# Performance work log

Hardware: AMD Instinct MI355X
Metric: run time of the kernel (lower is better)

Reference implementation:

```python
import jax, jax.numpy as jnp
import numpy as np

BLOCKS = (1, 2, 3, 4)      # (block_size, offset=0) from max_block_size=4
BLOCK_MULT = 12            # lcm(1,2,3,4)
DS = 4                     # downsample_factor
MAX_BS = 4                 # max block size (also pos_conv kernel size)
DIM = 512
VOCAB = 256


def _masked_mean(t, m, axis):
    # t: [..., L, D], m: [..., L] bool -> mean over axis with mask, 0 where empty
    mf = m[..., None].astype(t.dtype)
    num = jnp.sum(t * mf, axis=axis)
    tot = jnp.sum(mf, axis=axis)
    mean = num / jnp.clip(tot, 1.0)
    return jnp.where(tot == 0.0, jnp.zeros_like(mean), mean)


def setup_inputs() -> dict:
    key = jax.random.key(0)
    ks = jax.random.split(key, 8)
    B, S = 8, 2048
    return {
        "x": jax.random.randint(ks[0], (B, S), 0, VOCAB),
        "mask": jnp.ones((B, S), dtype=bool),
        "emb": jax.random.normal(ks[1], (VOCAB, DIM), jnp.float32) * 0.02,
        "dw_w": jax.random.normal(ks[2], (MAX_BS, 1, DIM), jnp.float32) * 0.1,   # depthwise kernel (W, I=1, O=DIM)
        "dw_b": jnp.zeros((DIM,), jnp.float32),
        "pw_w": jax.random.normal(ks[3], (1, DIM, DIM), jnp.float32) * 0.03,     # pointwise 1x1 conv
        "pw_b": jnp.zeros((DIM,), jnp.float32),
        "score_w": jax.random.normal(ks[4], (DIM, 1), jnp.float32) * 0.05,
        "score_b": jnp.zeros((1,), jnp.float32),
    }


def reference(x, mask, emb, dw_w, dw_b, pw_w, pw_b, score_w, score_b):
    B, S = x.shape
    D = DIM
    trunc = ((S + DS - 1) // DS) * DS  # next_divisible_length(S, DS); equals S here

    h = emb[x]                                              # [B,S,D]
    h = jnp.pad(h, ((0, 0), (0, MAX_BS - 1), (0, 0)))       # right pad for VALID conv
    dn = jax.lax.conv_dimension_numbers(h.shape, dw_w.shape, ('NWC', 'WIO', 'NWC'))
    h = jax.lax.conv_general_dilated(h, dw_w, (1,), 'VALID',
                                     dimension_numbers=dn,
                                     feature_group_count=D) + dw_b  # depthwise -> [B,S,D]
    h = jnp.einsum('bsd,de->bse', h, pw_w[0]) + pw_b                # pointwise

    # pad seq to multiple of lcm of block sizes
    Sp = ((h.shape[1] + BLOCK_MULT - 1) // BLOCK_MULT) * BLOCK_MULT
    pad = Sp - h.shape[1]
    h = jnp.pad(h, ((0, 0), (0, pad), (0, 0)))
    m = jnp.pad(mask.astype(bool), ((0, 0), (0, pad)), constant_values=False)

    reprs, rmasks = [], []
    for bsz in BLOCKS:  # fixed small set of block sizes (offset=0 for all)
        nb = Sp // bsz
        g = h.reshape(B, nb, bsz, D)
        mg = m.reshape(B, nb, bsz)
        r = _masked_mean(g, mg, axis=2)                       # [B,nb,D]
        reprs.append(jnp.repeat(r, bsz, axis=1))              # [B,Sp,D]
        rmasks.append(jnp.repeat(jnp.any(mg, axis=-1), bsz, axis=1))

    block_reprs = jnp.stack(reprs, axis=2)    # [B,Sp,M,D]
    block_masks = jnp.stack(rmasks, axis=2)   # [B,Sp,M]

    scores = (block_reprs @ score_w)[..., 0] + score_b[0]     # [B,Sp,M]
    max_neg = -jnp.finfo(scores.dtype).max
    scores = jnp.where(block_masks, scores, max_neg)
    scores = jnp.nan_to_num(jax.nn.softmax(scores, axis=2), nan=0.0)

    # consensus attention over positions
    sim = jnp.einsum('bim,bjm->bij', scores, scores)          # [B,Sp,Sp]
    cm = m[:, :, None] & m[:, None, :]
    sim = jnp.where(cm, sim, max_neg)
    attn = jnp.nan_to_num(jax.nn.softmax(sim, axis=-1), nan=0.0)
    scores = jnp.einsum('bij,bjm->bim', attn, scores)

    out = jnp.einsum('bsmd,bsm->bsd', block_reprs, scores)    # weighted combine
    out = out[:, :trunc]
    mt = m[:, :trunc]

    nl = trunc // DS
    xb = out.reshape(B, nl, DS, D)
    mb = mt.reshape(B, nl, DS)
    out = _masked_mean(xb, mb, axis=2)                        # [B, S/DS, D]
    out_mask = jnp.any(mb, axis=-1)
    return out, out_mask
```

## Files before the change

kernel.cpp:

```cpp
#include <hip/hip_runtime.h>
#include <stdint.h>
#include <stddef.h>

typedef __bf16 bf16_t;
typedef bf16_t bf16x4v __attribute__((ext_vector_type(4)));
typedef bf16_t bf16x8v __attribute__((ext_vector_type(8)));
typedef float  f32x4   __attribute__((ext_vector_type(4)));

#define NBATCH 8
#define SEQ    2048
#define DIM    512
#define SP     2052
#define NB2    1026
#define NB3    684
#define NB4    513
#define NL     512
#define NJC    8
#define JCH    257

static __device__ __forceinline__ f32x4 ldbf4(const bf16_t* p) {
  bf16x4v v = *(const bf16x4v*)p;
  f32x4 r;
  r.x = (float)v[0]; r.y = (float)v[1]; r.z = (float)v[2]; r.w = (float)v[3];
  return r;
}
static __device__ __forceinline__ void stbf4(bf16_t* p, f32x4 v) {
  bf16x4v o;
  o[0] = (bf16_t)v.x; o[1] = (bf16_t)v.y; o[2] = (bf16_t)v.z; o[3] = (bf16_t)v.w;
  *(bf16x4v*)p = o;
}

static __device__ __forceinline__ void gload_lds16(const void* g, void* l) {
  __builtin_amdgcn_global_load_lds(
      (const __attribute__((address_space(1))) void*)g,
      (__attribute__((address_space(3))) void*)l, 16, 0, 0);
}

#define GA_WT   256
#define GA_MASK 65
#define GA_A    (NBATCH * SEQ / 2)
__global__ __launch_bounds__(256) void kA_prep(
    const float* __restrict__ pw, bf16_t* __restrict__ Wt,
    const void* __restrict__ mraw, float* __restrict__ mask01,
    const int* __restrict__ x, const float* __restrict__ emb,
    const float* __restrict__ dww, const float* __restrict__ dwb,
    bf16_t* __restrict__ A) {
  const int bx = blockIdx.x, t = threadIdx.x;
  if (bx < GA_WT) {
    __shared__ float T[32][33];
    int ti = bx >> 4, tj = bx & 15;
    int r = t >> 3, c0 = (t & 7) * 4;
    f32x4 v = *(const f32x4*)(pw + (size_t)(ti * 32 + r) * DIM + tj * 32 + c0);
    T[c0 + 0][r] = v.x; T[c0 + 1][r] = v.y;
    T[c0 + 2][r] = v.z; T[c0 + 3][r] = v.w;
    __syncthreads();
    bf16x4v o;
    o[0] = (bf16_t)T[r][c0 + 0]; o[1] = (bf16_t)T[r][c0 + 1];
    o[2] = (bf16_t)T[r][c0 + 2]; o[3] = (bf16_t)T[r][c0 + 3];
    *(bf16x4v*)(Wt + (size_t)(tj * 32 + r) * DIM + ti * 32 + c0) = o;
    return;
  }
  if (bx < GA_WT + GA_MASK) {
    int idx = (bx - GA_WT) * 256 + t;
    if (idx >= NBATCH * SP) return;
    int b = idx / SP, s = idx - b * SP;
    const unsigned char* mb = (const unsigned char*)mraw;
    int u8 = 0;
#pragma unroll
    for (int i = 0; i < 64; i++)
      if ((i & 3) != 0 && mb[i] != 0) u8 = 1;
    float v = 0.f;
    if (s < SEQ) {
      int mi = b * SEQ + s;
      int nz = u8 ? (mb[mi] != 0) : (((const int*)mraw)[mi] != 0);
      v = nz ? 1.f : 0.f;
    }
    mask01[idx] = v;
    return;
  }
  int rp = bx - (GA_WT + GA_MASK);
  int row = rp * 2 + (t >> 7);
  int b = row >> 11, s = row & 2047;
  int d0 = (t & 127) * 4;
  f32x4 acc = *(const f32x4*)(dwb + d0);
#pragma unroll
  for (int tt = 0; tt < 4; tt++) {
    int sp = s + tt;
    if (sp < SEQ) {
      int v = x[b * SEQ + sp];
      f32x4 e = *(const f32x4*)(emb + (size_t)v * DIM + d0);
      f32x4 w = *(const f32x4*)(dww + tt * DIM + d0);
      acc += e * w;
    }
  }
  stbf4(A + (size_t)row * DIM + d0, acc);
}

#define BM 64
#define BN 128
#define BK 32
__global__ __launch_bounds__(256) void k2_gemm(
    const bf16_t* __restrict__ A, const bf16_t* __restrict__ Bt,
    const float* __restrict__ bias, bf16_t* __restrict__ H) {
  __shared__ __align__(16) bf16_t As[BM * BK];
  __shared__ __align__(16) bf16_t Bs[BN * BK];
  const int t = threadIdx.x;
  const int bid = blockIdx.x;
  const int xcd = bid & 7, loc = bid >> 3;
  const int mt = xcd * 32 + (loc >> 2);
  const int nt = loc & 3;
  const int m0 = mt * BM, n0 = nt * BN;
  const int lane = t & 63, wave = t >> 6;
  const int wm = (wave & 1) * 32, wn = (wave >> 1) * 64;
  const int mloc = lane & 15, quad = lane >> 4;

  f32x4 acc[2][4] = {};

  char* asd  = (char*)As + t * 16;
  char* bsd1 = (char*)Bs + t * 16;
  char* bsd2 = (char*)Bs + (t + 256) * 16;
  const int ar = t >> 2,           ak = (t & 3) * 8;
  const int br1 = t >> 2,          bk1 = (t & 3) * 8;
  const int br2 = (t + 256) >> 2,  bk2 = (t & 3) * 8;

  for (int k0 = 0; k0 < 512; k0 += BK) {
    gload_lds16(A + (size_t)(m0 + ar) * DIM + k0 + ak, asd);
    gload_lds16(Bt + (size_t)(n0 + br1) * DIM + k0 + bk1, bsd1);
    gload_lds16(Bt + (size_t)(n0 + br2) * DIM + k0 + bk2, bsd2);
    __syncthreads();
    bf16x8v af[2], bfr[4];
#pragma unroll
    for (int i = 0; i < 2; i++)
      af[i] = *(const bf16x8v*)&As[(wm + i * 16 + mloc) * BK + quad * 8];
#pragma unroll
    for (int i = 0; i < 4; i++)
      bfr[i] = *(const bf16x8v*)&Bs[(wn + i * 16 + mloc) * BK + quad * 8];
#pragma unroll
    for (int mi = 0; mi < 2; mi++)
#pragma unroll
      for (int ni = 0; ni < 4; ni++)
        acc[mi][ni] = __builtin_amdgcn_mfma_f32_16x16x32_bf16(
            af[mi], bfr[ni], acc[mi][ni], 0, 0, 0);
    __syncthreads();
  }
#pragma unroll
  for (int ni = 0; ni < 4; ni++) {
    int col = n0 + wn + ni * 16 + mloc;
    float bv = bias[col];
#pragma unroll
    for (int mi = 0; mi < 2; mi++) {
      int rbase = m0 + wm + mi * 16 + quad * 4;
#pragma unroll
      for (int r = 0; r < 4; r++)
        H[(size_t)(rbase + r) * DIM + col] = (bf16_t)(acc[mi][ni][r] + bv);
    }
  }
}

__global__ __launch_bounds__(128) void kB_levels(
    const bf16_t* __restrict__ H, const float* __restrict__ mask01,
    const float* __restrict__ sw, const float* __restrict__ sbp,
    bf16_t* __restrict__ R2, bf16_t* __restrict__ R3, bf16_t* __restrict__ R4,
    float* __restrict__ P) {
  const int b = blockIdx.x, c = blockIdx.y;
  const int s0 = c * 12;
  const int t = threadIdx.x;
  const int d0 = t * 4;
  const float sb = sbp[0];

  f32x4 h[12];
  float ms[12], p[12];
  f32x4 swv = *(const f32x4*)(sw + d0);
#pragma unroll
  for (int i = 0; i < 12; i++) {
    int s = s0 + i;
    ms[i] = mask01[b * SP + s];
    if (s < SEQ) {
      h[i] = ldbf4(H + ((size_t)b * SEQ + s) * DIM + d0);
    } else {
      h[i].x = h[i].y = h[i].z = h[i].w = 0.f;
    }
    p[i] = h[i].x * swv.x + h[i].y * swv.y + h[i].z * swv.z + h[i].w * swv.w;
  }
#pragma unroll
  for (int j = 0; j < 6; j++) {
    int i0 = 2 * j;
    float cc = ms[i0] + ms[i0 + 1];
    f32x4 sm = h[i0] * ms[i0] + h[i0 + 1] * ms[i0 + 1];
    float sc = cc > 0.f ? 1.f / cc : 0.f;
    stbf4(R2 + ((size_t)b * NB2 + (c * 6 + j)) * DIM + d0, sm * sc);
  }
#pragma unroll
  for (int j = 0; j < 4; j++) {
    int i0 = 3 * j;
    float cc = ms[i0] + ms[i0 + 1] + ms[i0 + 2];
    f32x4 sm = h[i0] * ms[i0] + h[i0 + 1] * ms[i0 + 1] + h[i0 + 2] * ms[i0 + 2];
    float sc = cc > 0.f ? 1.f / cc : 0.f;
    stbf4(R3 + ((size_t)b * NB3 + (c * 4 + j)) * DIM + d0, sm * sc);
  }
#pragma unroll
  for (int j = 0; j < 3; j++) {
    int i0 = 4 * j;
    float cc = ms[i0] + ms[i0 + 1] + ms[i0 + 2] + ms[i0 + 3];
    f32x4 sm = h[i0] * ms[i0] + h[i0 + 1] * ms[i0 + 1] +
               h[i0 + 2] * ms[i0 + 2] + h[i0 + 3] * ms[i0 + 3];
    float sc = cc > 0.f ? 1.f / cc : 0.f;
    stbf4(R4 + ((size_t)b * NB4 + (c * 3 + j)) * DIM + d0, sm * sc);
  }
#pragma unroll
  for (int off = 32; off > 0; off >>= 1)
#pragma unroll
    for (int i = 0; i < 12; i++) p[i] += __shfl_down(p[i], off);
  __shared__ float hsw[2][12];
  int lane = t & 63, wv = t >> 6;
  if (lane == 0)
#pragma unroll
    for (int i = 0; i < 12; i++) hsw[wv][i] = p[i];
  __syncthreads();
#define HSUM(i) (hsw[0][i] + hsw[1][i])
  if (t < 12) {
    int i = t;
    float m1 = ms[i];
    float v1 = HSUM(i) * m1 + sb;
    int i2 = i & ~1;
    float cc2 = ms[i2] + ms[i2 + 1];
    float s2 = HSUM(i2) * ms[i2] + HSUM(i2 + 1) * ms[i2 + 1];
    float v2 = (cc2 > 0.f ? s2 / cc2 : 0.f) + sb;
    int i3 = (i >= 9) ? 9 : (i >= 6) ? 6 : (i >= 3) ? 3 : 0;
    float cc3 = ms[i3] + ms[i3 + 1] + ms[i3 + 2];
    float s3 = HSUM(i3) * ms[i3] + HSUM(i3 + 1) * ms[i3 + 1] +
               HSUM(i3 + 2) * ms[i3 + 2];
    float v3 = (cc3 > 0.f ? s3 / cc3 : 0.f) + sb;
    int i4 = i & ~3;
    float cc4 = ms[i4] + ms[i4 + 1] + ms[i4 + 2] + ms[i4 + 3];
    float s4 = HSUM(i4) * ms[i4] + HSUM(i4 + 1) * ms[i4 + 1] +
               HSUM(i4 + 2) * ms[i4 + 2] + HSUM(i4 + 3) * ms[i4 + 3];
    float v4 = (cc4 > 0.f ? s4 / cc4 : 0.f) + sb;
    const float NEG = -3.0e38f;
    float a1 = m1 > 0.f ? v1 : NEG, a2 = cc2 > 0.f ? v2 : NEG;
    float a3 = cc3 > 0.f ? v3 : NEG, a4 = cc4 > 0.f ? v4 : NEG;
    float mx = fmaxf(fmaxf(a1, a2), fmaxf(a3, a4));
    f32x4 o;
    if (mx <= NEG) {
      o.x = o.y = o.z = o.w = 0.25f;
    } else {
      float e1 = m1 > 0.f ? __expf(v1 - mx) : 0.f;
      float e2 = cc2 > 0.f ? __expf(v2 - mx) : 0.f;
      float e3 = cc3 > 0.f ? __expf(v3 - mx) : 0.f;
      float e4 = cc4 > 0.f ? __expf(v4 - mx) : 0.f;
      float inv = 1.f / (e1 + e2 + e3 + e4);
      o.x = e1 * inv; o.y = e2 * inv; o.z = e3 * inv; o.w = e4 * inv;
    }
    *(f32x4*)(P + ((size_t)b * SP + s0 + i) * 4) = o;
  }
#undef HSUM
}

__global__ __launch_bounds__(128) void k5_attn(
    const float* __restrict__ P, const float* __restrict__ mask01,
    float* __restrict__ Wacc) {
  const int b = blockIdx.x, it = blockIdx.y, jc = blockIdx.z;
  const int t = threadIdx.x;
  __shared__ f32x4 Q[JCH];
  __shared__ float c2w[2];
  const int j0 = jc * JCH;
  const int len = (j0 + JCH <= SP) ? JCH : (SP - j0);
  float cnt0 = 0.f;
  for (int j = t; j < len; j += 128) {
    f32x4 q = *(const f32x4*)(P + ((size_t)b * SP + j0 + j) * 4);
    float mf = mask01[b * SP + j0 + j];
    if (mf == 0.f) {
      q.x = q.y = q.z = q.w = 0.f;
      cnt0 += 1.f;
    }
    Q[j] = q;
  }
#pragma unroll
  for (int off = 32; off > 0; off >>= 1) cnt0 += __shfl_down(cnt0, off);
  if ((t & 63) == 0) c2w[t >> 6] = cnt0;
  __syncthreads();
  const float nmask = c2w[0] + c2w[1];
  const int i = it * 128 + t;
  f32x4 qi = *(const f32x4*)(P + ((size_t)b * SP + i) * 4);
  float den = -nmask;
  f32x4 acc; acc.x = acc.y = acc.z = acc.w = 0.f;
  for (int j = 0; j < len; j++) {
    f32x4 pj = Q[j];
    float sim = qi.x * pj.x + qi.y * pj.y + qi.z * pj.z + qi.w * pj.w;
    float e = __expf(sim);
    den += e;
    acc += e * pj;
  }
  float* wp = Wacc + (((size_t)jc * NBATCH + b) * SEQ + i) * 5;
  wp[0] = acc.x; wp[1] = acc.y; wp[2] = acc.z; wp[3] = acc.w; wp[4] = den;
}

__global__ __launch_bounds__(128) void k6_out(
    const bf16_t* __restrict__ H, const bf16_t* __restrict__ R2,
    const bf16_t* __restrict__ R3, const bf16_t* __restrict__ R4,
    const float* __restrict__ mask01, const float* __restrict__ Wacc,
    float* __restrict__ out, float* __restrict__ omask) {
  const int b = blockIdx.x, l = blockIdx.y;
  const int t = threadIdx.x;
  const int d0 = t * 4;
  __shared__ f32x4 wsh[4];
  __shared__ float msh[4];
  if (t < 32) {
    int si = t >> 3, jc = t & 7;
    int s = l * 4 + si;
    const float* wp = Wacc + (((size_t)jc * NBATCH + b) * SEQ + s) * 5;
    float n0 = wp[0], n1 = wp[1], n2 = wp[2], n3 = wp[3], dn = wp[4];
#pragma unroll
    for (int off = 4; off > 0; off >>= 1) {
      n0 += __shfl_down(n0, off); n1 += __shfl_down(n1, off);
      n2 += __shfl_down(n2, off); n3 += __shfl_down(n3, off);
      dn += __shfl_down(dn, off);
    }
    if ((t & 7) == 0) {
      float inv = dn > 0.f ? 1.f / dn : 0.f;
      f32x4 w; w.x = n0 * inv; w.y = n1 * inv; w.z = n2 * inv; w.w = n3 * inv;
      wsh[si] = w;
      msh[si] = mask01[b * SP + s];
    }
  }
  __syncthreads();
  f32x4 o; o.x = o.y = o.z = o.w = 0.f;
  float cnt = 0.f;
#pragma unroll
  for (int si = 0; si < 4; si++) {
    int s = l * 4 + si;
    float m = msh[si];
    f32x4 w = wsh[si];
    f32x4 r1 = ldbf4(H + ((size_t)b * SEQ + s) * DIM + d0);
    f32x4 r2 = ldbf4(R2 + ((size_t)b * NB2 + (s >> 1)) * DIM + d0);
    f32x4 r3 = ldbf4(R3 + ((size_t)b * NB3 + (s / 3)) * DIM + d0);
    f32x4 r4 = ldbf4(R4 + ((size_t)b * NB4 + (s >> 2)) * DIM + d0);
    o += m * (w.x * r1 + w.y * r2 + w.z * r3 + w.w * r4);
    cnt += m;
  }
  float inv = cnt > 0.f ? 1.f / cnt : 0.f;
  o *= inv;
  *(f32x4*)(out + ((size_t)b * NL + l) * DIM + d0) = o;
  if (t == 0) omask[b * NL + l] = cnt > 0.f ? 1.f : 0.f;
}

extern "C" void kernel_launch(void* const* d_in, const int* in_sizes, int n_in,
                              void* d_out, int out_size, void* d_ws, size_t ws_size,
                              hipStream_t stream) {
  const int*   x    = (const int*)d_in[0];
  const void*  mraw = d_in[1];
  const float* emb  = (const float*)d_in[2];
  const float* dww  = (const float*)d_in[3];
  const float* dwb  = (const float*)d_in[4];
  const float* pw   = (const float*)d_in[5];
  const float* pwb  = (const float*)d_in[6];
  const float* sw   = (const float*)d_in[7];
  const float* sb   = (const float*)d_in[8];

  char* ws = (char*)d_ws;
  size_t off = 0;
  auto alloc = [&](size_t bytes) {
    size_t o = off;
    off = (off + bytes + 255) & ~(size_t)255;
    return o;
  };
  bf16_t* A    = (bf16_t*)(ws + alloc((size_t)NBATCH * SEQ * DIM * 2));
  bf16_t* H    = (bf16_t*)(ws + alloc((size_t)NBATCH * SEQ * DIM * 2));
  bf16_t* Wt   = (bf16_t*)(ws + alloc((size_t)DIM * DIM * 2));
  bf16_t* R2   = (bf16_t*)(ws + alloc((size_t)NBATCH * NB2 * DIM * 2));
  bf16_t* R3   = (bf16_t*)(ws + alloc((size_t)NBATCH * NB3 * DIM * 2));
  bf16_t* R4   = (bf16_t*)(ws + alloc((size_t)NBATCH * NB4 * DIM * 2));
  float* mask01 = (float*)(ws + alloc((size_t)NBATCH * SP * 4));
  float* P     = (float*)(ws + alloc((size_t)NBATCH * SP * 4 * 4));
  float* Wacc  = (float*)(ws + alloc((size_t)NJC * NBATCH * SEQ * 5 * 4));

  float* out   = (float*)d_out;
  float* omask = out + (size_t)NBATCH * NL * DIM;

  kA_prep<<<GA_WT + GA_MASK + GA_A, 256, 0, stream>>>(pw, Wt, mraw, mask01,
                                                      x, emb, dww, dwb, A);
  k2_gemm<<<1024, 256, 0, stream>>>(A, Wt, pwb, H);
  kB_levels<<<dim3(NBATCH, 171), 128, 0, stream>>>(H, mask01, sw, sb,
                                                   R2, R3, R4, P);
  k5_attn<<<dim3(NBATCH, 16, NJC), 128, 0, stream>>>(P, mask01, Wacc);
  k6_out<<<dim3(NBATCH, NL), 128, 0, stream>>>(H, R2, R3, R4, mask01, Wacc,
                                               out, omask);
}
```

Baseline: 141.5 us.

## Fuse all stages into one persistent kernel with grid-wide barriers

Replaces the five kernel launches with a single persistent kernel of 512 blocks. The stages (prep, GEMM, level pooling and scoring, attention plus output) are separated by atomic-counter grid barriers, and the barrier counter is zeroed with a memset before launch. The attention and output stages are merged so that each block handles 8 output rows over the full sequence kept in LDS. This removes the Wacc partial buffer and the cross-chunk reduction. The aim is to cut launch gaps and intermediate traffic, at the cost of needing all 512 blocks co-resident for the spin barriers, and of lower parallelism in the GEMM and attention stages.

```diff
diff --git a/kernel.cpp b/kernel.cpp
--- a/kernel.cpp
+++ b/kernel.cpp
@@ -15,8 +15,7 @@
 #define NB3    684
 #define NB4    513
 #define NL     512
-#define NJC    8
-#define JCH    257
+#define NBLK   512
 
 static __device__ __forceinline__ f32x4 ldbf4(const bf16_t* p) {
   bf16x4v v = *(const bf16x4v*)p;
@@ -36,19 +35,37 @@
       (__attribute__((address_space(3))) void*)l, 16, 0, 0);
 }
 
-#define GA_WT   256
-#define GA_MASK 65
-#define GA_A    (NBATCH * SEQ / 2)
-__global__ __launch_bounds__(256) void kA_prep(
-    const float* __restrict__ pw, bf16_t* __restrict__ Wt,
-    const void* __restrict__ mraw, float* __restrict__ mask01,
-    const int* __restrict__ x, const float* __restrict__ emb,
-    const float* __restrict__ dww, const float* __restrict__ dwb,
-    bf16_t* __restrict__ A) {
-  const int bx = blockIdx.x, t = threadIdx.x;
-  if (bx < GA_WT) {
-    __shared__ float T[32][33];
-    int ti = bx >> 4, tj = bx & 15;
+static __device__ __forceinline__ void gsync(int* bar, int target) {
+  __syncthreads();
+  if (threadIdx.x == 0) {
+    __threadfence();
+    atomicAdd(bar, 1);
+    while (atomicAdd(bar, 0) < target) __builtin_amdgcn_s_sleep(2);
+    __threadfence();
+  }
+  __syncthreads();
+}
+
+#define BM 64
+#define BN 128
+#define BK 32
+
+__global__ __launch_bounds__(256, 2) void mega(
+    const int* __restrict__ x, const void* __restrict__ mraw,
+    const float* __restrict__ emb, const float* __restrict__ dww,
+    const float* __restrict__ dwb, const float* __restrict__ pw,
+    const float* __restrict__ pwb, const float* __restrict__ sw,
+    const float* __restrict__ sbp,
+    bf16_t* __restrict__ A, bf16_t* __restrict__ H, bf16_t* __restrict__ Wt,
+    bf16_t* __restrict__ R2, bf16_t* __restrict__ R3, bf16_t* __restrict__ R4,
+    float* __restrict__ mask01, float* __restrict__ P,
+    float* __restrict__ out, float* __restrict__ omask, int* bar) {
+  __shared__ __align__(16) char smem[33024];
+  const int bid = blockIdx.x, t = threadIdx.x;
+
+  if (bid < 256) {
+    float (*T)[33] = (float(*)[33])smem;
+    int ti = bid >> 4, tj = bid & 15;
     int r = t >> 3, c0 = (t & 7) * 4;
     f32x4 v = *(const f32x4*)(pw + (size_t)(ti * 32 + r) * DIM + tj * 32 + c0);
     T[c0 + 0][r] = v.x; T[c0 + 1][r] = v.y;
@@ -58,290 +75,280 @@
     o[0] = (bf16_t)T[r][c0 + 0]; o[1] = (bf16_t)T[r][c0 + 1];
     o[2] = (bf16_t)T[r][c0 + 2]; o[3] = (bf16_t)T[r][c0 + 3];
     *(bf16x4v*)(Wt + (size_t)(tj * 32 + r) * DIM + ti * 32 + c0) = o;
-    return;
-  }
-  if (bx < GA_WT + GA_MASK) {
-    int idx = (bx - GA_WT) * 256 + t;
-    if (idx >= NBATCH * SP) return;
-    int b = idx / SP, s = idx - b * SP;
-    const unsigned char* mb = (const unsigned char*)mraw;
-    int u8 = 0;
-#pragma unroll
-    for (int i = 0; i < 64; i++)
-      if ((i & 3) != 0 && mb[i] != 0) u8 = 1;
-    float v = 0.f;
-    if (s < SEQ) {
-      int mi = b * SEQ + s;
-      int nz = u8 ? (mb[mi] != 0) : (((const int*)mraw)[mi] != 0);
-      v = nz ? 1.f : 0.f;
-    }
-    mask01[idx] = v;
-    return;
-  }
-  int rp = bx - (GA_WT + GA_MASK);
-  int row = rp * 2 + (t >> 7);
-  int b = row >> 11, s = row & 2047;
-  int d0 = (t & 127) * 4;
-  f32x4 acc = *(const f32x4*)(dwb + d0);
-#pragma unroll
-  for (int tt = 0; tt < 4; tt++) {
-    int sp = s + tt;
-    if (sp < SEQ) {
-      int v = x[b * SEQ + sp];
-      f32x4 e = *(const f32x4*)(emb + (size_t)v * DIM + d0);
-      f32x4 w = *(const f32x4*)(dww + tt * DIM + d0);
-      acc += e * w;
-    }
-  }
-  stbf4(A + (size_t)row * DIM + d0, acc);
-}
-
-#define BM 64
-#define BN 128
-#define BK 32
-__global__ __launch_bounds__(256) void k2_gemm(
-    const bf16_t* __restrict__ A, const bf16_t* __restrict__ Bt,
-    const float* __restrict__ bias, bf16_t* __restrict__ H) {
-  __shared__ __align__(16) bf16_t As[BM * BK];
-  __shared__ __align__(16) bf16_t Bs[BN * BK];
-  const int t = threadIdx.x;
-  const int bid = blockIdx.x;
-  const int xcd = bid & 7, loc = bid >> 3;
-  const int mt = xcd * 32 + (loc >> 2);
-  const int nt = loc & 3;
-  const int m0 = mt * BM, n0 = nt * BN;
-  const int lane = t & 63, wave = t >> 6;
-  const int wm = (wave & 1) * 32, wn = (wave >> 1) * 64;
-  const int mloc = lane & 15, quad = lane >> 4;
-
-  f32x4 acc[2][4] = {};
-
-  char* asd  = (char*)As + t * 16;
-  char* bsd1 = (char*)Bs + t * 16;
-  char* bsd2 = (char*)Bs + (t + 256) * 16;
-  const int ar = t >> 2,           ak = (t & 3) * 8;
-  const int br1 = t >> 2,          bk1 = (t & 3) * 8;
-  const int br2 = (t + 256) >> 2,  bk2 = (t & 3) * 8;
-
-  for (int k0 = 0; k0 < 512; k0 += BK) {
-    gload_lds16(A + (size_t)(m0 + ar) * DIM + k0 + ak, asd);
-    gload_lds16(Bt + (size_t)(n0 + br1) * DIM + k0 + bk1, bsd1);
-    gload_lds16(Bt + (size_t)(n0 + br2) * DIM + k0 + bk2, bsd2);
+  } else if (bid < 321) {
+    int idx = (bid - 256) * 256 + t;
+    if (idx < NBATCH * SP) {
+      int b = idx / SP, s = idx - b * SP;
+      const unsigned char* mb = (const unsigned char*)mraw;
+      int u8 = 0;
+#pragma unroll
+      for (int i = 0; i < 64; i++)
+        if ((i & 3) != 0 && mb[i] != 0) u8 = 1;
+      float v = 0.f;
+      if (s < SEQ) {
+        int mi = b * SEQ + s;
+        int nz = u8 ? (mb[mi] != 0) : (((const int*)mraw)[mi] != 0);
+        v = nz ? 1.f : 0.f;
+      }
+      mask01[idx] = v;
+    }
+  }
+  {
+    int d0 = (t & 127) * 4;
+    int rsel = t >> 7;
+#pragma unroll 4
+    for (int i = 0; i < 16; i++) {
+      int row = (bid * 16 + i) * 2 + rsel;
+      int b = row >> 11, s = row & 2047;
+      f32x4 acc = *(const f32x4*)(dwb + d0);
+#pragma unroll
+      for (int tt = 0; tt < 4; tt++) {
+        int sp = s + tt;
+        if (sp < SEQ) {
+          int v = x[b * SEQ + sp];
+          f32x4 e = *(const f32x4*)(emb + (size_t)v * DIM + d0);
+          f32x4 w = *(const f32x4*)(dww + tt * DIM + d0);
+          acc += e * w;
+        }
+      }
+      stbf4(A + (size_t)row * DIM + d0, acc);
+    }
+  }
+  gsync(bar, NBLK);
+
+  {
+    bf16_t* As = (bf16_t*)smem;
+    bf16_t* Bs = As + BM * BK;
+    const int lane = t & 63, wave = t >> 6;
+    const int wm = (wave & 1) * 32, wn = (wave >> 1) * 64;
+    const int mloc = lane & 15, quad = lane >> 4;
+    char* asd  = (char*)As + t * 16;
+    char* bsd1 = (char*)Bs + t * 16;
+    char* bsd2 = (char*)Bs + (t + 256) * 16;
+    const int ar = t >> 2, ak = (t & 3) * 8;
+    const int br2 = (t + 256) >> 2;
+#pragma unroll 1
+    for (int half = 0; half < 2; half++) {
+      int tile = bid + half * 512;
+      int xcd = tile & 7, loc = tile >> 3;
+      int mt = xcd * 32 + (loc >> 2), nt = loc & 3;
+      int m0 = mt * BM, n0 = nt * BN;
+      f32x4 acc[2][4] = {};
+      for (int k0 = 0; k0 < 512; k0 += BK) {
+        gload_lds16(A + (size_t)(m0 + ar) * DIM + k0 + ak, asd);
+        gload_lds16(Wt + (size_t)(n0 + ar) * DIM + k0 + ak, bsd1);
+        gload_lds16(Wt + (size_t)(n0 + br2) * DIM + k0 + ak, bsd2);
+        __syncthreads();
+        bf16x8v af[2], bfr[4];
+#pragma unroll
+        for (int i = 0; i < 2; i++)
+          af[i] = *(const bf16x8v*)&As[(wm + i * 16 + mloc) * BK + quad * 8];
+#pragma unroll
+        for (int i = 0; i < 4; i++)
+          bfr[i] = *(const bf16x8v*)&Bs[(wn + i * 16 + mloc) * BK + quad * 8];
+#pragma unroll
+        for (int mi = 0; mi < 2; mi++)
+#pragma unroll
+          for (int ni = 0; ni < 4; ni++)
+            acc[mi][ni] = __builtin_amdgcn_mfma_f32_16x16x32_bf16(
+                af[mi], bfr[ni], acc[mi][ni], 0, 0, 0);
+        __syncthreads();
+      }
+#pragma unroll
+      for (int ni = 0; ni < 4; ni++) {
+        int col = n0 + wn + ni * 16 + mloc;
+        float bv = pwb[col];
+#pragma unroll
+        for (int mi = 0; mi < 2; mi++) {
+          int rbase = m0 + wm + mi * 16 + quad * 4;
+#pragma unroll
+          for (int r = 0; r < 4; r++)
+            H[(size_t)(rbase + r) * DIM + col] = (bf16_t)(acc[mi][ni][r] + bv);
+        }
+      }
+    }
+  }
+  gsync(bar, 2 * NBLK);
+
+  {
+    float* hsw = (float*)smem;
+    const int h = t >> 7, t1 = t & 127, wv = (t >> 6) & 1, lane = t & 63;
+    const float sb = sbp[0];
+#pragma unroll 1
+    for (int pass = 0; pass < 2; pass++) {
+      int unit = pass * 1024 + bid * 2 + h;
+      bool act = unit < 1368;
+      int uu = act ? unit : 0;
+      int b = uu / 171, c = uu - b * 171;
+      int s0 = c * 12, d0 = t1 * 4;
+      f32x4 hh[12];
+      float ms[12], p[12];
+      f32x4 swv = *(const f32x4*)(sw + d0);
+#pragma unroll
+      for (int i = 0; i < 12; i++) {
+        int s = s0 + i;
+        ms[i] = mask01[b * SP + s];
+        if (s < SEQ) {
+          hh[i] = ldbf4(H + ((size_t)b * SEQ + s) * DIM + d0);
+        } else {
+          hh[i].x = hh[i].y = hh[i].z = hh[i].w = 0.f;
+        }
+        p[i] = hh[i].x * swv.x + hh[i].y * swv.y + hh[i].z * swv.z +
+               hh[i].w * swv.w;
+      }
+      if (act) {
+#pragma unroll
+        for (int j = 0; j < 6; j++) {
+          int i0 = 2 * j;
+          float cc = ms[i0] + ms[i0 + 1];
+          f32x4 sm = hh[i0] * ms[i0] + hh[i0 + 1] * ms[i0 + 1];
+          float sc = cc > 0.f ? 1.f / cc : 0.f;
+          stbf4(R2 + ((size_t)b * NB2 + (c * 6 + j)) * DIM + d0, sm * sc);
+        }
+#pragma unroll
+        for (int j = 0; j < 4; j++) {
+          int i0 = 3 * j;
+          float cc = ms[i0] + ms[i0 + 1] + ms[i0 + 2];
+          f32x4 sm = hh[i0] * ms[i0] + hh[i0 + 1] * ms[i0 + 1] +
+                     hh[i0 + 2] * ms[i0 + 2];
+          float sc = cc > 0.f ? 1.f / cc : 0.f;
+          stbf4(R3 + ((size_t)b * NB3 + (c * 4 + j)) * DIM + d0, sm * sc);
+        }
+#pragma unroll
+        for (int j = 0; j < 3; j++) {
+          int i0 = 4 * j;
+          float cc = ms[i0] + ms[i0 + 1] + ms[i0 + 2] + ms[i0 + 3];
+          f32x4 sm = hh[i0] * ms[i0] + hh[i0 + 1] * ms[i0 + 1] +
+                     hh[i0 + 2] * ms[i0 + 2] + hh[i0 + 3] * ms[i0 + 3];
+          float sc = cc > 0.f ? 1.f / cc : 0.f;
+          stbf4(R4 + ((size_t)b * NB4 + (c * 3 + j)) * DIM + d0, sm * sc);
+        }
+      }
+#pragma unroll
+      for (int off = 32; off > 0; off >>= 1)
+#pragma unroll
+        for (int i = 0; i < 12; i++) p[i] += __shfl_down(p[i], off);
+      if (lane == 0)
+#pragma unroll
+        for (int i = 0; i < 12; i++) hsw[(h * 2 + wv) * 12 + i] = p[i];
+      __syncthreads();
+#define HSUM(i) (hsw[(h * 2) * 12 + (i)] + hsw[(h * 2 + 1) * 12 + (i)])
+      if (act && t1 < 12) {
+        int i = t1;
+        float m1 = ms[i];
+        float v1 = HSUM(i) * m1 + sb;
+        int i2 = i & ~1;
+        float cc2 = ms[i2] + ms[i2 + 1];
+        float s2 = HSUM(i2) * ms[i2] + HSUM(i2 + 1) * ms[i2 + 1];
+        float v2 = (cc2 > 0.f ? s2 / cc2 : 0.f) + sb;
+        int i3 = (i >= 9) ? 9 : (i >= 6) ? 6 : (i >= 3) ? 3 : 0;
+        float cc3 = ms[i3] + ms[i3 + 1] + ms[i3 + 2];
+        float s3 = HSUM(i3) * ms[i3] + HSUM(i3 + 1) * ms[i3 + 1] +
+                   HSUM(i3 + 2) * ms[i3 + 2];
+        float v3 = (cc3 > 0.f ? s3 / cc3 : 0.f) + sb;
+        int i4 = i & ~3;
+        float cc4 = ms[i4] + ms[i4 + 1] + ms[i4 + 2] + ms[i4 + 3];
+        float s4 = HSUM(i4) * ms[i4] + HSUM(i4 + 1) * ms[i4 + 1] +
+                   HSUM(i4 + 2) * ms[i4 + 2] + HSUM(i4 + 3) * ms[i4 + 3];
+        float v4 = (cc4 > 0.f ? s4 / cc4 : 0.f) + sb;
+        const float NEG = -3.0e38f;
+        float a1 = m1 > 0.f ? v1 : NEG, a2 = cc2 > 0.f ? v2 : NEG;
+        float a3 = cc3 > 0.f ? v3 : NEG, a4 = cc4 > 0.f ? v4 : NEG;
+        float mx = fmaxf(fmaxf(a1, a2), fmaxf(a3, a4));
+        f32x4 o;
+        if (mx <= NEG) {
+          o.x = o.y = o.z = o.w = 0.25f;
+        } else {
+          float e1 = m1 > 0.f ? __expf(v1 - mx) : 0.f;
+          float e2 = cc2 > 0.f ? __expf(v2 - mx) : 0.f;
+          float e3 = cc3 > 0.f ? __expf(v3 - mx) : 0.f;
+          float e4 = cc4 > 0.f ? __expf(v4 - mx) : 0.f;
+          float inv = 1.f / (e1 + e2 + e3 + e4);
+          o.x = e1 * inv; o.y = e2 * inv; o.z = e3 * inv; o.w = e4 * inv;
+        }
+        *(f32x4*)(P + ((size_t)b * SP + s0 + i) * 4) = o;
+      }
+#undef HSUM
+      __syncthreads();
+    }
+  }
+  gsync(bar, 3 * NBLK);
+
+  {
+    f32x4* Qs = (f32x4*)smem;
+    float* nmp  = (float*)(smem + 32832);
+    f32x4* wshl = (f32x4*)(smem + 32848);
+    float* mshl = (float*)(smem + 32912);
+    const int b = bid >> 6, lbase = (bid & 63) * 8;
+    if (t == 0) *nmp = 0.f;
     __syncthreads();
-    bf16x8v af[2], bfr[4];
-#pragma unroll
-    for (int i = 0; i < 2; i++)
-      af[i] = *(const bf16x8v*)&As[(wm + i * 16 + mloc) * BK + quad * 8];
-#pragma unroll
-    for (int i = 0; i < 4; i++)
-      bfr[i] = *(const bf16x8v*)&Bs[(wn + i * 16 + mloc) * BK + quad * 8];
-#pragma unroll
-    for (int mi = 0; mi < 2; mi++)
-#pragma unroll
-      for (int ni = 0; ni < 4; ni++)
-        acc[mi][ni] = __builtin_amdgcn_mfma_f32_16x16x32_bf16(
-            af[mi], bfr[ni], acc[mi][ni], 0, 0, 0);
+    for (int j = t; j < SP; j += 256) {
+      f32x4 q = *(const f32x4*)(P + ((size_t)b * SP + j) * 4);
+      float mf = mask01[b * SP + j];
+      if (mf == 0.f) {
+        q.x = q.y = q.z = q.w = 0.f;
+        atomicAdd(nmp, 1.f);
+      }
+      Qs[j] = q;
+    }
     __syncthreads();
-  }
-#pragma unroll
-  for (int ni = 0; ni < 4; ni++) {
-    int col = n0 + wn + ni * 16 + mloc;
-    float bv = bias[col];
-#pragma unroll
-    for (int mi = 0; mi < 2; mi++) {
-      int rbase = m0 + wm + mi * 16 + quad * 4;
-#pragma unroll
-      for (int r = 0; r < 4; r++)
-        H[(size_t)(rbase + r) * DIM + col] = (bf16_t)(acc[mi][ni][r] + bv);
-    }
-  }
-}
-
-__global__ __launch_bounds__(128) void kB_levels(
-    const bf16_t* __restrict__ H, const float* __restrict__ mask01,
-    const float* __restrict__ sw, const float* __restrict__ sbp,
-    bf16_t* __restrict__ R2, bf16_t* __restrict__ R3, bf16_t* __restrict__ R4,
-    float* __restrict__ P) {
-  const int b = blockIdx.x, c = blockIdx.y;
-  const int s0 = c * 12;
-  const int t = threadIdx.x;
-  const int d0 = t * 4;
-  const float sb = sbp[0];
-
-  f32x4 h[12];
-  float ms[12], p[12];
-  f32x4 swv = *(const f32x4*)(sw + d0);
-#pragma unroll
-  for (int i = 0; i < 12; i++) {
-    int s = s0 + i;
-    ms[i] = mask01[b * SP + s];
-    if (s < SEQ) {
-      h[i] = ldbf4(H + ((size_t)b * SEQ + s) * DIM + d0);
-    } else {
-      h[i].x = h[i].y = h[i].z = h[i].w = 0.f;
-    }
-    p[i] = h[i].x * swv.x + h[i].y * swv.y + h[i].z * swv.z + h[i].w * swv.w;
-  }
-#pragma unroll
-  for (int j = 0; j < 6; j++) {
-    int i0 = 2 * j;
-    float cc = ms[i0] + ms[i0 + 1];
-    f32x4 sm = h[i0] * ms[i0] + h[i0 + 1] * ms[i0 + 1];
-    float sc = cc > 0.f ? 1.f / cc : 0.f;
-    stbf4(R2 + ((size_t)b * NB2 + (c * 6 + j)) * DIM + d0, sm * sc);
-  }
-#pragma unroll
-  for (int j = 0; j < 4; j++) {
-    int i0 = 3 * j;
-    float cc = ms[i0] + ms[i0 + 1] + ms[i0 + 2];
-    f32x4 sm = h[i0] * ms[i0] + h[i0 + 1] * ms[i0 + 1] + h[i0 + 2] * ms[i0 + 2];
-    float sc = cc > 0.f ? 1.f / cc : 0.f;
-    stbf4(R3 + ((size_t)b * NB3 + (c * 4 + j)) * DIM + d0, sm * sc);
-  }
-#pragma unroll
-  for (int j = 0; j < 3; j++) {
-    int i0 = 4 * j;
-    float cc = ms[i0] + ms[i0 + 1] + ms[i0 + 2] + ms[i0 + 3];
-    f32x4 sm = h[i0] * ms[i0] + h[i0 + 1] * ms[i0 + 1] +
-               h[i0 + 2] * ms[i0 + 2] + h[i0 + 3] * ms[i0 + 3];
-    float sc = cc > 0.f ? 1.f / cc : 0.f;
-    stbf4(R4 + ((size_t)b * NB4 + (c * 3 + j)) * DIM + d0, sm * sc);
-  }
-#pragma unroll
-  for (int off = 32; off > 0; off >>= 1)
-#pragma unroll
-    for (int i = 0; i < 12; i++) p[i] += __shfl_down(p[i], off);
-  __shared__ float hsw[2][12];
-  int lane = t & 63, wv = t >> 6;
-  if (lane == 0)
-#pragma unroll
-    for (int i = 0; i < 12; i++) hsw[wv][i] = p[i];
-  __syncthreads();
-#define HSUM(i) (hsw[0][i] + hsw[1][i])
-  if (t < 12) {
-    int i = t;
-    float m1 = ms[i];
-    float v1 = HSUM(i) * m1 + sb;
-    int i2 = i & ~1;
-    float cc2 = ms[i2] + ms[i2 + 1];
-    float s2 = HSUM(i2) * ms[i2] + HSUM(i2 + 1) * ms[i2 + 1];
-    float v2 = (cc2 > 0.f ? s2 / cc2 : 0.f) + sb;
-    int i3 = (i >= 9) ? 9 : (i >= 6) ? 6 : (i >= 3) ? 3 : 0;
-    float cc3 = ms[i3] + ms[i3 + 1] + ms[i3 + 2];
-    float s3 = HSUM(i3) * ms[i3] + HSUM(i3 + 1) * ms[i3 + 1] +
-               HSUM(i3 + 2) * ms[i3 + 2];
-    float v3 = (cc3 > 0.f ? s3 / cc3 : 0.f) + sb;
-    int i4 = i & ~3;
-    float cc4 = ms[i4] + ms[i4 + 1] + ms[i4 + 2] + ms[i4 + 3];
-    float s4 = HSUM(i4) * ms[i4] + HSUM(i4 + 1) * ms[i4 + 1] +
-               HSUM(i4 + 2) * ms[i4 + 2] + HSUM(i4 + 3) * ms[i4 + 3];
-    float v4 = (cc4 > 0.f ? s4 / cc4 : 0.f) + sb;
-    const float NEG = -3.0e38f;
-    float a1 = m1 > 0.f ? v1 : NEG, a2 = cc2 > 0.f ? v2 : NEG;
-    float a3 = cc3 > 0.f ? v3 : NEG, a4 = cc4 > 0.f ? v4 : NEG;
-    float mx = fmaxf(fmaxf(a1, a2), fmaxf(a3, a4));
-    f32x4 o;
-    if (mx <= NEG) {
-      o.x = o.y = o.z = o.w = 0.25f;
-    } else {
-      float e1 = m1 > 0.f ? __expf(v1 - mx) : 0.f;
-      float e2 = cc2 > 0.f ? __expf(v2 - mx) : 0.f;
-      float e3 = cc3 > 0.f ? __expf(v3 - mx) : 0.f;
-      float e4 = cc4 > 0.f ? __expf(v4 - mx) : 0.f;
-      float inv = 1.f / (e1 + e2 + e3 + e4);
-      o.x = e1 * inv; o.y = e2 * inv; o.z = e3 * inv; o.w = e4 * inv;
-    }
-    *(f32x4*)(P + ((size_t)b * SP + s0 + i) * 4) = o;
-  }
-#undef HSUM
-}
-
-__global__ __launch_bounds__(128) void k5_attn(
-    const float* __restrict__ P, const float* __restrict__ mask01,
-    float* __restrict__ Wacc) {
-  const int b = blockIdx.x, it = blockIdx.y, jc = blockIdx.z;
-  const int t = threadIdx.x;
-  __shared__ f32x4 Q[JCH];
-  __shared__ float c2w[2];
-  const int j0 = jc * JCH;
-  const int len = (j0 + JCH <= SP) ? JCH : (SP - j0);
-  float cnt0 = 0.f;
-  for (int j = t; j < len; j += 128) {
-    f32x4 q = *(const f32x4*)(P + ((size_t)b * SP + j0 + j) * 4);
-    float mf = mask01[b * SP + j0 + j];
-    if (mf == 0.f) {
-      q.x = q.y = q.z = q.w = 0.f;
-      cnt0 += 1.f;
-    }
-    Q[j] = q;
-  }
-#pragma unroll
-  for (int off = 32; off > 0; off >>= 1) cnt0 += __shfl_down(cnt0, off);
-  if ((t & 63) == 0) c2w[t >> 6] = cnt0;
-  __syncthreads();
-  const float nmask = c2w[0] + c2w[1];
-  const int i = it * 128 + t;
-  f32x4 qi = *(const f32x4*)(P + ((size_t)b * SP + i) * 4);
-  float den = -nmask;
-  f32x4 acc; acc.x = acc.y = acc.z = acc.w = 0.f;
-  for (int j = 0; j < len; j++) {
-    f32x4 pj = Q[j];
-    float sim = qi.x * pj.x + qi.y * pj.y + qi.z * pj.z + qi.w * pj.w;
-    float e = __expf(sim);
-    den += e;
-    acc += e * pj;
-  }
-  float* wp = Wacc + (((size_t)jc * NBATCH + b) * SEQ + i) * 5;
-  wp[0] = acc.x; wp[1] = acc.y; wp[2] = acc.z; wp[3] = acc.w; wp[4] = den;
-}
-
-__global__ __launch_bounds__(128) void k6_out(
-    const bf16_t* __restrict__ H, const bf16_t* __restrict__ R2,
-    const bf16_t* __restrict__ R3, const bf16_t* __restrict__ R4,
-    const float* __restrict__ mask01, const float* __restrict__ Wacc,
-    float* __restrict__ out, float* __restrict__ omask) {
-  const int b = blockIdx.x, l = blockIdx.y;
-  const int t = threadIdx.x;
-  const int d0 = t * 4;
-  __shared__ f32x4 wsh[4];
-  __shared__ float msh[4];
-  if (t < 32) {
-    int si = t >> 3, jc = t & 7;
-    int s = l * 4 + si;
-    const float* wp = Wacc + (((size_t)jc * NBATCH + b) * SEQ + s) * 5;
-    float n0 = wp[0], n1 = wp[1], n2 = wp[2], n3 = wp[3], dn = wp[4];
-#pragma unroll
-    for (int off = 4; off > 0; off >>= 1) {
-      n0 += __shfl_down(n0, off); n1 += __shfl_down(n1, off);
-      n2 += __shfl_down(n2, off); n3 += __shfl_down(n3, off);
-      dn += __shfl_down(dn, off);
-    }
-    if ((t & 7) == 0) {
-      float inv = dn > 0.f ? 1.f / dn : 0.f;
-      f32x4 w; w.x = n0 * inv; w.y = n1 * inv; w.z = n2 * inv; w.w = n3 * inv;
-      wsh[si] = w;
-      msh[si] = mask01[b * SP + s];
-    }
-  }
-  __syncthreads();
-  f32x4 o; o.x = o.y = o.z = o.w = 0.f;
-  float cnt = 0.f;
-#pragma unroll
-  for (int si = 0; si < 4; si++) {
-    int s = l * 4 + si;
-    float m = msh[si];
-    f32x4 w = wsh[si];
-    f32x4 r1 = ldbf4(H + ((size_t)b * SEQ + s) * DIM + d0);
-    f32x4 r2 = ldbf4(R2 + ((size_t)b * NB2 + (s >> 1)) * DIM + d0);
-    f32x4 r3 = ldbf4(R3 + ((size_t)b * NB3 + (s / 3)) * DIM + d0);
-    f32x4 r4 = ldbf4(R4 + ((size_t)b * NB4 + (s >> 2)) * DIM + d0);
-    o += m * (w.x * r1 + w.y * r2 + w.z * r3 + w.w * r4);
-    cnt += m;
-  }
-  float inv = cnt > 0.f ? 1.f / cnt : 0.f;
-  o *= inv;
-  *(f32x4*)(out + ((size_t)b * NL + l) * DIM + d0) = o;
-  if (t == 0) omask[b * NL + l] = cnt > 0.f ? 1.f : 0.f;
+    const float nmv = *nmp;
+    const int w = t >> 6, lane = t & 63;
+#pragma unroll 1
+    for (int li = 0; li < 8; li++) {
+      int l = lbase + li;
+      int s = l * 4 + w;
+      f32x4 qi = Qs[s];
+      f32x4 acc; acc.x = acc.y = acc.z = acc.w = 0.f;
+      float den = 0.f;
+      for (int j = lane; j < SP; j += 64) {
+        f32x4 pj = Qs[j];
+        float e = __expf(qi.x * pj.x + qi.y * pj.y + qi.z * pj.z +
+                         qi.w * pj.w);
+        den += e;
+        acc += e * pj;
+      }
+#pragma unroll
+      for (int off = 32; off > 0; off >>= 1) {
+        acc.x += __shfl_down(acc.x, off);
+        acc.y += __shfl_down(acc.y, off);
+        acc.z += __shfl_down(acc.z, off);
+        acc.w += __shfl_down(acc.w, off);
+        den   += __shfl_down(den, off);
+      }
+      if (lane == 0) {
+        den -= nmv;
+        float inv = den > 0.f ? 1.f / den : 0.f;
+        f32x4 wv4; wv4.x = acc.x * inv; wv4.y = acc.y * inv;
+        wv4.z = acc.z * inv; wv4.w = acc.w * inv;
+        wshl[w] = wv4;
+        mshl[w] = mask01[b * SP + s];
+      }
+      __syncthreads();
+      if (t < 128) {
+        int d0 = t * 4;
+        f32x4 o; o.x = o.y = o.z = o.w = 0.f;
+        float cnt = 0.f;
+#pragma unroll
+        for (int si = 0; si < 4; si++) {
+          int ss = l * 4 + si;
+          float m = mshl[si];
+          f32x4 wv4 = wshl[si];
+          f32x4 r1 = ldbf4(H + ((size_t)b * SEQ + ss) * DIM + d0);
+          f32x4 r2 = ldbf4(R2 + ((size_t)b * NB2 + (ss >> 1)) * DIM + d0);
+          f32x4 r3 = ldbf4(R3 + ((size_t)b * NB3 + (ss / 3)) * DIM + d0);
+          f32x4 r4 = ldbf4(R4 + ((size_t)b * NB4 + (ss >> 2)) * DIM + d0);
+          o += m * (wv4.x * r1 + wv4.y * r2 + wv4.z * r3 + wv4.w * r4);
+          cnt += m;
+        }
+        float inv = cnt > 0.f ? 1.f / cnt : 0.f;
+        o *= inv;
+        *(f32x4*)(out + ((size_t)b * NL + l) * DIM + d0) = o;
+        if (t == 0) omask[b * NL + l] = cnt > 0.f ? 1.f : 0.f;
+      }
+      __syncthreads();
+    }
+  }
 }
 
 extern "C" void kernel_launch(void* const* d_in, const int* in_sizes, int n_in,
@@ -364,6 +371,7 @@
     off = (off + bytes + 255) & ~(size_t)255;
     return o;
   };
+  int*   bar   = (int*)(ws + alloc(256));
   bf16_t* A    = (bf16_t*)(ws + alloc((size_t)NBATCH * SEQ * DIM * 2));
   bf16_t* H    = (bf16_t*)(ws + alloc((size_t)NBATCH * SEQ * DIM * 2));
   bf16_t* Wt   = (bf16_t*)(ws + alloc((size_t)DIM * DIM * 2));
@@ -372,17 +380,12 @@
   bf16_t* R4   = (bf16_t*)(ws + alloc((size_t)NBATCH * NB4 * DIM * 2));
   float* mask01 = (float*)(ws + alloc((size_t)NBATCH * SP * 4));
   float* P     = (float*)(ws + alloc((size_t)NBATCH * SP * 4 * 4));
-  float* Wacc  = (float*)(ws + alloc((size_t)NJC * NBATCH * SEQ * 5 * 4));
 
   float* out   = (float*)d_out;
   float* omask = out + (size_t)NBATCH * NL * DIM;
 
-  kA_prep<<<GA_WT + GA_MASK + GA_A, 256, 0, stream>>>(pw, Wt, mraw, mask01,
-                                                      x, emb, dww, dwb, A);
-  k2_gemm<<<1024, 256, 0, stream>>>(A, Wt, pwb, H);
-  kB_levels<<<dim3(NBATCH, 171), 128, 0, stream>>>(H, mask01, sw, sb,
-                                                   R2, R3, R4, P);
-  k5_attn<<<dim3(NBATCH, 16, NJC), 128, 0, stream>>>(P, mask01, Wacc);
-  k6_out<<<dim3(NBATCH, NL), 128, 0, stream>>>(H, R2, R3, R4, mask01, Wacc,
-                                               out, omask);
-}
+  hipMemsetAsync(bar, 0, 256, stream);
+  mega<<<NBLK, 256, 0, stream>>>(x, mraw, emb, dww, dwb, pw, pwb, sw, sb,
+                                 A, H, Wt, R2, R3, R4, mask01, P,
+                                 out, omask, bar);
+}
```

Result: slower. 319.1 us (+125.5%).

## Fuse consensus attention and output combine into one kernel with full-row reductions

Applied to the files above, without the earlier changes.

The separate attention kernel, which wrote per-chunk partial sums to a workspace, and the output-combine kernel are merged into one kernel. Each block loads the whole batch row of block scores into LDS as structure-of-arrays, computes each query's full softmax row with a wave-wide shuffle reduction, and then does the weighted combine and downsample mean directly. This drops one launch and the partial-sum round trip through global memory. In exchange the grid is much smaller (512 blocks), every block redundantly loads the full row of P, and the j-loop is serialized per wave. The GEMM loader index cleanup is cosmetic.

```diff
diff --git a/kernel.cpp b/kernel.cpp
--- a/kernel.cpp
+++ b/kernel.cpp
@@ -15,8 +15,6 @@
 #define NB3    684
 #define NB4    513
 #define NL     512
-#define NJC    8
-#define JCH    257
 
 static __device__ __forceinline__ f32x4 ldbf4(const bf16_t* p) {
   bf16x4v v = *(const bf16x4v*)p;
@@ -119,14 +117,13 @@
   char* asd  = (char*)As + t * 16;
   char* bsd1 = (char*)Bs + t * 16;
   char* bsd2 = (char*)Bs + (t + 256) * 16;
-  const int ar = t >> 2,           ak = (t & 3) * 8;
-  const int br1 = t >> 2,          bk1 = (t & 3) * 8;
-  const int br2 = (t + 256) >> 2,  bk2 = (t & 3) * 8;
+  const int ar = t >> 2, ak = (t & 3) * 8;
+  const int br2 = (t + 256) >> 2;
 
   for (int k0 = 0; k0 < 512; k0 += BK) {
     gload_lds16(A + (size_t)(m0 + ar) * DIM + k0 + ak, asd);
-    gload_lds16(Bt + (size_t)(n0 + br1) * DIM + k0 + bk1, bsd1);
-    gload_lds16(Bt + (size_t)(n0 + br2) * DIM + k0 + bk2, bsd2);
+    gload_lds16(Bt + (size_t)(n0 + ar) * DIM + k0 + ak, bsd1);
+    gload_lds16(Bt + (size_t)(n0 + br2) * DIM + k0 + ak, bsd2);
     __syncthreads();
     bf16x8v af[2], bfr[4];
 #pragma unroll
@@ -256,92 +253,89 @@
 #undef HSUM
 }
 
-__global__ __launch_bounds__(128) void k5_attn(
+__global__ __launch_bounds__(256) void k56_attn_out(
     const float* __restrict__ P, const float* __restrict__ mask01,
-    float* __restrict__ Wacc) {
-  const int b = blockIdx.x, it = blockIdx.y, jc = blockIdx.z;
+    const bf16_t* __restrict__ H, const bf16_t* __restrict__ R2,
+    const bf16_t* __restrict__ R3, const bf16_t* __restrict__ R4,
+    float* __restrict__ out, float* __restrict__ omask) {
+  __shared__ float Px[SP], Py[SP], Pz[SP], Pw[SP];
+  __shared__ f32x4 ws4[32];
+  __shared__ float msk[32];
+  __shared__ float c4w[4];
+  const int b = blockIdx.x, lbase = blockIdx.y * 8;
   const int t = threadIdx.x;
-  __shared__ f32x4 Q[JCH];
-  __shared__ float c2w[2];
-  const int j0 = jc * JCH;
-  const int len = (j0 + JCH <= SP) ? JCH : (SP - j0);
+  const int w = t >> 6, lane = t & 63;
+
   float cnt0 = 0.f;
-  for (int j = t; j < len; j += 128) {
-    f32x4 q = *(const f32x4*)(P + ((size_t)b * SP + j0 + j) * 4);
-    float mf = mask01[b * SP + j0 + j];
+  for (int j = t; j < SP; j += 256) {
+    f32x4 q = *(const f32x4*)(P + ((size_t)b * SP + j) * 4);
+    float mf = mask01[b * SP + j];
     if (mf == 0.f) {
       q.x = q.y = q.z = q.w = 0.f;
       cnt0 += 1.f;
     }
-    Q[j] = q;
+    Px[j] = q.x; Py[j] = q.y; Pz[j] = q.z; Pw[j] = q.w;
   }
 #pragma unroll
   for (int off = 32; off > 0; off >>= 1) cnt0 += __shfl_down(cnt0, off);
-  if ((t & 63) == 0) c2w[t >> 6] = cnt0;
+  if (lane == 0) c4w[w] = cnt0;
   __syncthreads();
-  const float nmask = c2w[0] + c2w[1];
-  const int i = it * 128 + t;
-  f32x4 qi = *(const f32x4*)(P + ((size_t)b * SP + i) * 4);
-  float den = -nmask;
-  f32x4 acc; acc.x = acc.y = acc.z = acc.w = 0.f;
-  for (int j = 0; j < len; j++) {
-    f32x4 pj = Q[j];
-    float sim = qi.x * pj.x + qi.y * pj.y + qi.z * pj.z + qi.w * pj.w;
-    float e = __expf(sim);
-    den += e;
-    acc += e * pj;
-  }
-  float* wp = Wacc + (((size_t)jc * NBATCH + b) * SEQ + i) * 5;
-  wp[0] = acc.x; wp[1] = acc.y; wp[2] = acc.z; wp[3] = acc.w; wp[4] = den;
-}
-
-__global__ __launch_bounds__(128) void k6_out(
-    const bf16_t* __restrict__ H, const bf16_t* __restrict__ R2,
-    const bf16_t* __restrict__ R3, const bf16_t* __restrict__ R4,
-    const float* __restrict__ mask01, const float* __restrict__ Wacc,
-    float* __restrict__ out, float* __restrict__ omask) {
-  const int b = blockIdx.x, l = blockIdx.y;
-  const int t = threadIdx.x;
-  const int d0 = t * 4;
-  __shared__ f32x4 wsh[4];
-  __shared__ float msh[4];
-  if (t < 32) {
-    int si = t >> 3, jc = t & 7;
-    int s = l * 4 + si;
-    const float* wp = Wacc + (((size_t)jc * NBATCH + b) * SEQ + s) * 5;
-    float n0 = wp[0], n1 = wp[1], n2 = wp[2], n3 = wp[3], dn = wp[4];
-#pragma unroll
-    for (int off = 4; off > 0; off >>= 1) {
-      n0 += __shfl_down(n0, off); n1 += __shfl_down(n1, off);
-      n2 += __shfl_down(n2, off); n3 += __shfl_down(n3, off);
-      dn += __shfl_down(dn, off);
-    }
-    if ((t & 7) == 0) {
-      float inv = dn > 0.f ? 1.f / dn : 0.f;
-      f32x4 w; w.x = n0 * inv; w.y = n1 * inv; w.z = n2 * inv; w.w = n3 * inv;
-      wsh[si] = w;
-      msh[si] = mask01[b * SP + s];
+  const float nmv = c4w[0] + c4w[1] + c4w[2] + c4w[3];
+
+#pragma unroll 1
+  for (int k = 0; k < 8; k++) {
+    int sl = w * 8 + k;
+    int s = lbase * 4 + sl;
+    float qx = Px[s], qy = Py[s], qz = Pz[s], qw = Pw[s];
+    float ax = 0.f, ay = 0.f, az = 0.f, aw = 0.f, den = 0.f;
+    for (int j = lane; j < SP; j += 64) {
+      float px = Px[j], py = Py[j], pz = Pz[j], pw4 = Pw[j];
+      float e = __expf(qx * px + qy * py + qz * pz + qw * pw4);
+      den += e;
+      ax += e * px; ay += e * py; az += e * pz; aw += e * pw4;
+    }
+#pragma unroll
+    for (int off = 32; off > 0; off >>= 1) {
+      ax += __shfl_down(ax, off); ay += __shfl_down(ay, off);
+      az += __shfl_down(az, off); aw += __shfl_down(aw, off);
+      den += __shfl_down(den, off);
+    }
+    if (lane == 0) {
+      den -= nmv;
+      float inv = den > 0.f ? 1.f / den : 0.f;
+      f32x4 wv4; wv4.x = ax * inv; wv4.y = ay * inv;
+      wv4.z = az * inv; wv4.w = aw * inv;
+      ws4[sl] = wv4;
+      msk[sl] = mask01[b * SP + s];
     }
   }
   __syncthreads();
-  f32x4 o; o.x = o.y = o.z = o.w = 0.f;
-  float cnt = 0.f;
-#pragma unroll
-  for (int si = 0; si < 4; si++) {
-    int s = l * 4 + si;
-    float m = msh[si];
-    f32x4 w = wsh[si];
-    f32x4 r1 = ldbf4(H + ((size_t)b * SEQ + s) * DIM + d0);
-    f32x4 r2 = ldbf4(R2 + ((size_t)b * NB2 + (s >> 1)) * DIM + d0);
-    f32x4 r3 = ldbf4(R3 + ((size_t)b * NB3 + (s / 3)) * DIM + d0);
-    f32x4 r4 = ldbf4(R4 + ((size_t)b * NB4 + (s >> 2)) * DIM + d0);
-    o += m * (w.x * r1 + w.y * r2 + w.z * r3 + w.w * r4);
-    cnt += m;
-  }
-  float inv = cnt > 0.f ? 1.f / cnt : 0.f;
-  o *= inv;
-  *(f32x4*)(out + ((size_t)b * NL + l) * DIM + d0) = o;
-  if (t == 0) omask[b * NL + l] = cnt > 0.f ? 1.f : 0.f;
+
+#pragma unroll 1
+  for (int p = 0; p < 4; p++) {
+    int ll = p * 2 + (t >> 7);
+    int l = lbase + ll;
+    int d0 = (t & 127) * 4;
+    f32x4 o; o.x = o.y = o.z = o.w = 0.f;
+    float cnt = 0.f;
+#pragma unroll
+    for (int si = 0; si < 4; si++) {
+      int sl = ll * 4 + si;
+      int s = l * 4 + si;
+      float m = msk[sl];
+      f32x4 wv4 = ws4[sl];
+      f32x4 r1 = ldbf4(H + ((size_t)b * SEQ + s) * DIM + d0);
+      f32x4 r2 = ldbf4(R2 + ((size_t)b * NB2 + (s >> 1)) * DIM + d0);
+      f32x4 r3 = ldbf4(R3 + ((size_t)b * NB3 + (s / 3)) * DIM + d0);
+      f32x4 r4 = ldbf4(R4 + ((size_t)b * NB4 + (s >> 2)) * DIM + d0);
+      o += m * (wv4.x * r1 + wv4.y * r2 + wv4.z * r3 + wv4.w * r4);
+      cnt += m;
+    }
+    float inv = cnt > 0.f ? 1.f / cnt : 0.f;
+    o *= inv;
+    *(f32x4*)(out + ((size_t)b * NL + l) * DIM + d0) = o;
+    if ((t & 127) == 0) omask[b * NL + l] = cnt > 0.f ? 1.f : 0.f;
+  }
 }
 
 extern "C" void kernel_launch(void* const* d_in, const int* in_sizes, int n_in,
@@ -372,7 +366,6 @@
   bf16_t* R4   = (bf16_t*)(ws + alloc((size_t)NBATCH * NB4 * DIM * 2));
   float* mask01 = (float*)(ws + alloc((size_t)NBATCH * SP * 4));
   float* P     = (float*)(ws + alloc((size_t)NBATCH * SP * 4 * 4));
-  float* Wacc  = (float*)(ws + alloc((size_t)NJC * NBATCH * SEQ * 5 * 4));
 
   float* out   = (float*)d_out;
   float* omask = out + (size_t)NBATCH * NL * DIM;
@@ -382,7 +375,6 @@
   k2_gemm<<<1024, 256, 0, stream>>>(A, Wt, pwb, H);
   kB_levels<<<dim3(NBATCH, 171), 128, 0, stream>>>(H, mask01, sw, sb,
                                                    R2, R3, R4, P);
-  k5_attn<<<dim3(NBATCH, 16, NJC), 128, 0, stream>>>(P, mask01, Wacc);
-  k6_out<<<dim3(NBATCH, NL), 128, 0, stream>>>(H, R2, R3, R4, mask01, Wacc,
-                                               out, omask);
-}
+  k56_attn_out<<<dim3(NBATCH, 64), 256, 0, stream>>>(P, mask01, H, R2, R3, R4,
+                                                     out, omask);
+}
```

Result: slower. 153.1 us (+8.2%).
